# Performance work log

Hardware: AMD Instinct MI355X
Metric: run time of the kernel (lower is better)

The kernel has to match this reference:

```python
import jax, jax.numpy as jnp
import numpy as np

EPS = 1e-5  # config.layer_norm_epsilon

def setup_inputs() -> dict:
    key = jax.random.key(0)
    ks = jax.random.split(key, 8)
    B, S, D, BOT, N = 8, 2048, 1024, 400, 25
    x = jax.random.normal(ks[0], (B, S, D), dtype=jnp.float32)
    alphas = jax.random.uniform(ks[1], (N,), dtype=jnp.float32) / N
    W_down_all = jax.random.normal(ks[2], (N, BOT, D), dtype=jnp.float32) * 0.02
    W_up_all = jax.random.normal(ks[3], (N, D, BOT), dtype=jnp.float32) * 0.02
    b_down_all = jax.random.normal(ks[4], (N, BOT), dtype=jnp.float32) * 0.02
    b_up_all = jax.random.normal(ks[5], (N, D), dtype=jnp.float32) * 0.02
    W_ln_all = 1.0 + jax.random.normal(ks[6], (N, D), dtype=jnp.float32) * 0.02
    b_ln_all = jax.random.normal(ks[7], (N, D), dtype=jnp.float32) * 0.02
    return {"x": x, "alphas": alphas, "W_down_all": W_down_all, "W_up_all": W_up_all,
            "b_down_all": b_down_all, "b_up_all": b_up_all,
            "W_ln_all": W_ln_all, "b_ln_all": b_ln_all}

def reference(x, alphas, W_down_all, W_up_all, b_down_all, b_up_all, W_ln_all, b_ln_all):
    # Superposition: alpha-weighted sum of all adapters' parameters
    # (original python loop over 25 adapters -> single einsum per tensor).
    W_down = jnp.einsum('n,nbd->bd', alphas, W_down_all)  # [BOT, D]
    W_up   = jnp.einsum('n,ndb->db', alphas, W_up_all)    # [D, BOT]
    W_ln   = jnp.einsum('n,nd->d',  alphas, W_ln_all)     # [D]
    b_ln   = jnp.einsum('n,nd->d',  alphas, b_ln_all)     # [D]
    # b_up / b_down are merged in the original too but passed with bias=None: unused.

    # FAdapter: F.layer_norm with normalized_shape = x.shape[1:], i.e. normalize
    # jointly over (seq, embd) per batch element; ln weight/bias broadcast over seq.
    mu = jnp.mean(x, axis=(1, 2), keepdims=True)
    var = jnp.mean(jnp.square(x - mu), axis=(1, 2), keepdims=True)
    x_ = (x - mu) * jax.lax.rsqrt(var + EPS) * W_ln + b_ln  # [B,S,D]

    h = jax.nn.relu(jnp.einsum('bsd,od->bso', x_, W_down))  # [B,S,BOT], no bias
    x_ = jnp.einsum('bso,do->bsd', h, W_up)                 # [B,S,D],   no bias
    return x + x_
```

## Files before the change

kernel.cpp:

```cpp
#include <hip/hip_runtime.h>
#include <stdint.h>

#define NB   8
#define SS   2048
#define DD   1024
#define BOT  400
#define BOTP 512
#define NAD  25
#define LN_EPS 1e-5f
#define NCH  128

typedef __attribute__((ext_vector_type(8))) short bf8_t;
typedef __attribute__((ext_vector_type(4))) float fx4;

__device__ __forceinline__ unsigned short f2bf(float f) {
  unsigned int u = __float_as_uint(f);
  u = (u + 0x7FFFu + ((u >> 16) & 1u)) >> 16;
  return (unsigned short)u;
}
__device__ __forceinline__ uint32_t cvtpk(float lo, float hi) {
  uint32_t r;
  asm("v_cvt_pk_bf16_f32 %0, %1, %2" : "=v"(r) : "v"(lo), "v"(hi));
  return r;
}

__device__ __forceinline__ void gload16(void* lds, const void* g) {
  __builtin_amdgcn_global_load_lds(
      (const __attribute__((address_space(1))) void*)(uintptr_t)g,
      (__attribute__((address_space(3))) void*)(uint32_t)(uintptr_t)lds,
      16, 0, 0);
}

__global__ __launch_bounds__(256) void mixstats_kernel(
    const float* __restrict__ alphas,
    const float* __restrict__ WdAll, const float* __restrict__ WuAll,
    const float* __restrict__ wlnAll, const float* __restrict__ blnAll,
    const float* __restrict__ x,
    unsigned short* __restrict__ Wd, unsigned short* __restrict__ Wu,
    float* __restrict__ wln, float* __restrict__ bln,
    float* __restrict__ partials)
{
  const int tid = threadIdx.x;
  const int bid = blockIdx.x;

  if (bid >= 920) {
    const int g = bid - 920;
    const int b = g >> 7, c = g & 127;
    const float4* xb = (const float4*)(x + (size_t)b * SS * DD) + (size_t)c * 4096;
    float s = 0.f, q = 0.f;
#pragma unroll 4
    for (int i = tid; i < 4096; i += 256) {
      float4 v = xb[i];
      s += v.x + v.y + v.z + v.w;
      q += v.x * v.x + v.y * v.y + v.z * v.z + v.w * v.w;
    }
#pragma unroll
    for (int off = 32; off > 0; off >>= 1) { s += __shfl_down(s, off); q += __shfl_down(q, off); }
    __shared__ float red[8];
    const int wave = tid >> 6, lane = tid & 63;
    if (!lane) { red[wave] = s; red[wave + 4] = q; }
    __syncthreads();
    if (!tid) {
      partials[(b * NCH + c) * 2]     = red[0] + red[1] + red[2] + red[3];
      partials[(b * NCH + c) * 2 + 1] = red[4] + red[5] + red[6] + red[7];
    }
    return;
  }

  __shared__ float a[NAD];
  if (tid < NAD) a[tid] = alphas[tid];
  __syncthreads();

  if (bid < 800) {
    const int g = (bid < 400 ? bid : bid - 400) * 256 + tid;
    const float4* src = (const float4*)(bid < 400 ? WdAll : WuAll) + g;
    float4 vals[NAD];
#pragma unroll
    for (int n = 0; n < NAD; ++n) vals[n] = src[(size_t)n * 102400];
    float4 acc = {0.f, 0.f, 0.f, 0.f};
#pragma unroll
    for (int n = 0; n < NAD; ++n) {
      acc.x += a[n] * vals[n].x; acc.y += a[n] * vals[n].y;
      acc.z += a[n] * vals[n].z; acc.w += a[n] * vals[n].w;
    }
    uint2 pk = { cvtpk(acc.x, acc.y), cvtpk(acc.z, acc.w) };
    if (bid < 400) {
      *(uint2*)(Wd + (size_t)g * 4) = pk;
    } else {
      const int d = g / 100, bg = g - d * 100;
      *(uint2*)(Wu + (size_t)d * BOTP + bg * 4) = pk;
    }
  } else if (bid < 808) {
    const int i = (bid - 800) * 256 + tid;
    const float* src = (i < DD) ? wlnAll : blnAll;
    const int j = (i < DD) ? i : (i - DD);
    float v[NAD];
#pragma unroll
    for (int n = 0; n < NAD; ++n) v[n] = src[(size_t)n * DD + j];
    float s = 0.f;
#pragma unroll
    for (int n = 0; n < NAD; ++n) s += a[n] * v[n];
    if (i < DD) wln[j] = s; else bln[j] = s;
  } else if (bid < 864) {
    const int t = (bid - 808) * 256 + tid;
    int4 z = {0, 0, 0, 0};
    *(int4*)(Wd + 400 * 1024 + (size_t)t * 8) = z;
  } else {
    const int t = (bid - 864) * 256 + tid;
    const int row = t / 14, c8 = t - row * 14;
    int4 z = {0, 0, 0, 0};
    *(int4*)(Wu + (size_t)row * BOTP + 400 + c8 * 8) = z;
  }
}

__global__ __launch_bounds__(256) void gemm1(
    const float* __restrict__ x, const unsigned short* __restrict__ Wdm,
    const float* __restrict__ partials, const float* __restrict__ wln,
    const float* __restrict__ bln, unsigned short* __restrict__ H)
{
  __shared__ char smraw[32768];
  unsigned short* As = (unsigned short*)smraw;
  unsigned short* Bs = (unsigned short*)(smraw + 8192);
  float* s1 = (float*)(smraw + 16384);
  float* s2 = (float*)(smraw + 20480);

  const int tid = threadIdx.x, wave = tid >> 6, lane = tid & 63;
  const int wr = wave >> 1, wc = wave & 1;
  const int bcol = blockIdx.x & 3, brow = blockIdx.x >> 2;
  const int b = brow >> 4;

  double sd = 0.0, qd = 0.0;
#pragma unroll 8
  for (int i = 0; i < NCH; ++i) {
    sd += partials[(b * NCH + i) * 2];
    qd += partials[(b * NCH + i) * 2 + 1];
  }
  const float mu  = (float)(sd * (1.0 / 2097152.0));
  const float var = (float)(qd * (1.0 / 2097152.0)) - mu * mu;
  const float rs  = rsqrtf(var + LN_EPS);
  for (int c = tid; c < DD; c += 256) {
    const float v1 = rs * wln[c];
    s1[c] = v1; s2[c] = bln[c] - mu * v1;
  }

  const float* Ab = x + (size_t)(brow * 128) * DD;
  const unsigned short* Bb = Wdm + (size_t)(bcol * 128) * DD;
  const int row2 = tid >> 1;
  const int c16  = (tid & 1) * 16;

  auto loadA = [&](int k0, float4* xr) {
    const float* p = Ab + (size_t)row2 * DD + k0 + c16;
    xr[0] = *(const float4*)p;     xr[1] = *(const float4*)(p + 4);
    xr[2] = *(const float4*)(p + 8); xr[3] = *(const float4*)(p + 12);
  };
  auto writeA = [&](int k0, const float4* xr) {
    const float4 wA = *(const float4*)&s1[k0 + c16],      wB = *(const float4*)&s1[k0 + c16 + 4];
    const float4 wC = *(const float4*)&s1[k0 + c16 + 8],  wD = *(const float4*)&s1[k0 + c16 + 12];
    const float4 bA = *(const float4*)&s2[k0 + c16],      bB = *(const float4*)&s2[k0 + c16 + 4];
    const float4 bC = *(const float4*)&s2[k0 + c16 + 8],  bD = *(const float4*)&s2[k0 + c16 + 12];
    uint4 p0, p1;
    p0.x = cvtpk(xr[0].x * wA.x + bA.x, xr[0].y * wA.y + bA.y);
    p0.y = cvtpk(xr[0].z * wA.z + bA.z, xr[0].w * wA.w + bA.w);
    p0.z = cvtpk(xr[1].x * wB.x + bB.x, xr[1].y * wB.y + bB.y);
    p0.w = cvtpk(xr[1].z * wB.z + bB.z, xr[1].w * wB.w + bB.w);
    p1.x = cvtpk(xr[2].x * wC.x + bC.x, xr[2].y * wC.y + bC.y);
    p1.y = cvtpk(xr[2].z * wC.z + bC.z, xr[2].w * wC.w + bC.w);
    p1.z = cvtpk(xr[3].x * wD.x + bD.x, xr[3].y * wD.y + bD.y);
    p1.w = cvtpk(xr[3].z * wD.z + bD.z, xr[3].w * wD.w + bD.w);
    *(uint4*)&As[row2 * 32 + c16]     = p0;
    *(uint4*)&As[row2 * 32 + c16 + 8] = p1;
  };
  auto stageB = [&](int k0) {
#pragma unroll
    for (int i = 0; i < 2; ++i) {
      const int basee = (i * 256 + wave * 64) * 8;
      const int e   = basee + lane * 8;
      const int row = e >> 5, col = e & 31;
      gload16(&Bs[basee], Bb + (size_t)row * DD + k0 + col);
    }
  };

  fx4 acc[4][4] = {};
  auto compute = [&]() {
    bf8_t af[4], bf[4];
    const int hi8 = (lane >> 4) * 8;
#pragma unroll
    for (int m = 0; m < 4; ++m)
      af[m] = *(const bf8_t*)&As[(wr * 64 + m * 16 + (lane & 15)) * 32 + hi8];
#pragma unroll
    for (int n = 0; n < 4; ++n)
      bf[n] = *(const bf8_t*)&Bs[(wc * 64 + n * 16 + (lane & 15)) * 32 + hi8];
#pragma unroll
    for (int m = 0; m < 4; ++m)
#pragma unroll
      for (int n = 0; n < 4; ++n)
        acc[m][n] = __builtin_amdgcn_mfma_f32_16x16x32_bf16(af[m], bf[n], acc[m][n], 0, 0, 0);
  };

  float4 xrA[4], xrB[4];
  loadA(0, xrA); stageB(0); loadA(32, xrB);
  __syncthreads();
  writeA(0, xrA);
  __syncthreads();
#pragma unroll 1
  for (int t2 = 0; t2 < 16; ++t2) {
    {
      const int t = t2 * 2;
      compute();
      __syncthreads();
      if (t < 31) {
        stageB((t + 1) * 32);
        writeA((t + 1) * 32, xrB);
        if (t + 2 < 32) loadA((t + 2) * 32, xrA);
      }
      __syncthreads();
    }
    {
      const int t = t2 * 2 + 1;
      compute();
      __syncthreads();
      if (t < 31) {
        stageB((t + 1) * 32);
        writeA((t + 1) * 32, xrA);
        if (t + 2 < 32) loadA((t + 2) * 32, xrB);
      }
      __syncthreads();
    }
  }

  unsigned short* Hs = (unsigned short*)smraw;
  const int r0l = wr * 64 + ((lane >> 4) << 2);
  const int c0l = wc * 64 + (lane & 15);
#pragma unroll
  for (int m = 0; m < 4; ++m)
#pragma unroll
    for (int n = 0; n < 4; ++n)
#pragma unroll
      for (int j = 0; j < 4; ++j) {
        float v = acc[m][n][j];
        Hs[(r0l + m * 16 + j) * 128 + (c0l + n * 16)] = f2bf(v > 0.f ? v : 0.f);
      }
  __syncthreads();
  const size_t outbase = (size_t)(brow * 128) * BOTP + (size_t)bcol * 128;
#pragma unroll
  for (int i = 0; i < 8; ++i) {
    const int idx = i * 256 + tid;
    const int row = idx >> 4, colg = idx & 15;
    *(int4*)(H + outbase + (size_t)row * BOTP + colg * 8) = *(const int4*)&Hs[row * 128 + colg * 8];
  }
}

__global__ __launch_bounds__(256) void gemm2(
    const unsigned short* __restrict__ A, const unsigned short* __restrict__ Bm,
    const float* __restrict__ Xres, float* __restrict__ out)
{
  __shared__ unsigned short As[128 * 32];
  __shared__ unsigned short Bs[128 * 32];
  const int tid = threadIdx.x, wave = tid >> 6, lane = tid & 63;
  const int wr = wave >> 1, wc = wave & 1;
  const int bcol = blockIdx.x & 7, brow = blockIdx.x >> 3;
  const unsigned short* Ab = A + (size_t)(brow * 128) * BOTP;
  const unsigned short* Bb = Bm + (size_t)(bcol * 128) * BOTP;

  fx4 acc[4][4] = {};
  for (int k0 = 0; k0 < 512; k0 += 32) {
#pragma unroll
    for (int i = 0; i < 2; ++i) {
      const int basee = (i * 256 + wave * 64) * 8;
      const int e   = basee + lane * 8;
      const int row = e >> 5, col = e & 31;
      gload16(&As[basee], Ab + (size_t)row * BOTP + k0 + col);
      gload16(&Bs[basee], Bb + (size_t)row * BOTP + k0 + col);
    }
    __syncthreads();
    bf8_t af[4], bf[4];
    const int hi8 = (lane >> 4) * 8;
#pragma unroll
    for (int m = 0; m < 4; ++m)
      af[m] = *(const bf8_t*)&As[(wr * 64 + m * 16 + (lane & 15)) * 32 + hi8];
#pragma unroll
    for (int n = 0; n < 4; ++n)
      bf[n] = *(const bf8_t*)&Bs[(wc * 64 + n * 16 + (lane & 15)) * 32 + hi8];
#pragma unroll
    for (int m = 0; m < 4; ++m)
#pragma unroll
      for (int n = 0; n < 4; ++n)
        acc[m][n] = __builtin_amdgcn_mfma_f32_16x16x32_bf16(af[m], bf[n], acc[m][n], 0, 0, 0);
    __syncthreads();
  }

  const int r0 = brow * 128 + wr * 64 + ((lane >> 4) << 2);
  const int c0 = bcol * 128 + wc * 64 + (lane & 15);
#pragma unroll
  for (int m = 0; m < 4; ++m)
#pragma unroll
    for (int n = 0; n < 4; ++n)
#pragma unroll
      for (int j = 0; j < 4; ++j) {
        const size_t off = (size_t)(r0 + m * 16 + j) * DD + (c0 + n * 16);
        out[off] = acc[m][n][j] + Xres[off];
      }
}

extern "C" void kernel_launch(void* const* d_in, const int* in_sizes, int n_in,
                              void* d_out, int out_size, void* d_ws, size_t ws_size,
                              hipStream_t stream)
{
  const float* x      = (const float*)d_in[0];
  const float* alphas = (const float*)d_in[1];
  const float* WdAll  = (const float*)d_in[2];
  const float* WuAll  = (const float*)d_in[3];
  const float* wlnAll = (const float*)d_in[6];
  const float* blnAll = (const float*)d_in[7];
  float* out = (float*)d_out;

  char* ws = (char*)d_ws;
  unsigned short* Wd  = (unsigned short*)ws;
  unsigned short* Wu  = (unsigned short*)(ws + (1u << 20));
  float* wln          = (float*)(ws + (2u << 20));
  float* bln          = wln + DD;
  float* partials     = bln + DD;
  unsigned short* h   = (unsigned short*)(ws + (3u << 20));

  mixstats_kernel<<<1944, 256, 0, stream>>>(alphas, WdAll, WuAll, wlnAll, blnAll, x,
                                            Wd, Wu, wln, bln, partials);
  gemm1<<<512, 256, 0, stream>>>(x, Wd, partials, wln, bln, h);
  gemm2<<<1024, 256, 0, stream>>>(h, Wu, x, out);
}
```

Baseline: 275.2 us.

## Split layernorm into separate bf16 pass and unify GEMMs with K=64 tiles

LayerNorm application is moved out of gemm1 into a standalone kernel that writes normalized x as bf16 to workspace. Both GEMMs become one templated kernel with 64-wide K tiles, XCD-aware block remapping, and an LDS-staged coalesced epilogue for the fp32 residual add. Sched barriers force all loads to issue before the arithmetic in the mixing and stats kernels. The extra pass writes and rereads about 32 MB of bf16 activations, traded for a simpler GEMM1 inner loop and fewer barriers per K step. The old register double-buffering of A is dropped.

```diff
diff --git a/kernel.cpp b/kernel.cpp
--- a/kernel.cpp
+++ b/kernel.cpp
@@ -47,12 +47,15 @@
     const int g = bid - 920;
     const int b = g >> 7, c = g & 127;
     const float4* xb = (const float4*)(x + (size_t)b * SS * DD) + (size_t)c * 4096;
+    float4 v[16];
+#pragma unroll
+    for (int i = 0; i < 16; ++i) v[i] = xb[i * 256 + tid];
+    __builtin_amdgcn_sched_barrier(0);
     float s = 0.f, q = 0.f;
-#pragma unroll 4
-    for (int i = tid; i < 4096; i += 256) {
-      float4 v = xb[i];
-      s += v.x + v.y + v.z + v.w;
-      q += v.x * v.x + v.y * v.y + v.z * v.z + v.w * v.w;
+#pragma unroll
+    for (int i = 0; i < 16; ++i) {
+      s += v[i].x + v[i].y + v[i].z + v[i].w;
+      q += v[i].x * v[i].x + v[i].y * v[i].y + v[i].z * v[i].z + v[i].w * v[i].w;
     }
 #pragma unroll
     for (int off = 32; off > 0; off >>= 1) { s += __shfl_down(s, off); q += __shfl_down(q, off); }
@@ -77,6 +80,7 @@
     float4 vals[NAD];
 #pragma unroll
     for (int n = 0; n < NAD; ++n) vals[n] = src[(size_t)n * 102400];
+    __builtin_amdgcn_sched_barrier(0);
     float4 acc = {0.f, 0.f, 0.f, 0.f};
 #pragma unroll
     for (int n = 0; n < NAD; ++n) {
@@ -97,6 +101,7 @@
     float v[NAD];
 #pragma unroll
     for (int n = 0; n < NAD; ++n) v[n] = src[(size_t)n * DD + j];
+    __builtin_amdgcn_sched_barrier(0);
     float s = 0.f;
 #pragma unroll
     for (int n = 0; n < NAD; ++n) s += a[n] * v[n];
@@ -113,22 +118,11 @@
   }
 }
 
-__global__ __launch_bounds__(256) void gemm1(
-    const float* __restrict__ x, const unsigned short* __restrict__ Wdm,
+__global__ __launch_bounds__(256) void norm_kernel(const float* __restrict__ x,
     const float* __restrict__ partials, const float* __restrict__ wln,
-    const float* __restrict__ bln, unsigned short* __restrict__ H)
-{
-  __shared__ char smraw[32768];
-  unsigned short* As = (unsigned short*)smraw;
-  unsigned short* Bs = (unsigned short*)(smraw + 8192);
-  float* s1 = (float*)(smraw + 16384);
-  float* s2 = (float*)(smraw + 20480);
-
-  const int tid = threadIdx.x, wave = tid >> 6, lane = tid & 63;
-  const int wr = wave >> 1, wc = wave & 1;
-  const int bcol = blockIdx.x & 3, brow = blockIdx.x >> 2;
-  const int b = brow >> 4;
-
+    const float* __restrict__ bln, unsigned short* __restrict__ xn)
+{
+  const int b = blockIdx.y;
   double sd = 0.0, qd = 0.0;
 #pragma unroll 8
   for (int i = 0; i < NCH; ++i) {
@@ -138,168 +132,126 @@
   const float mu  = (float)(sd * (1.0 / 2097152.0));
   const float var = (float)(qd * (1.0 / 2097152.0)) - mu * mu;
   const float rs  = rsqrtf(var + LN_EPS);
-  for (int c = tid; c < DD; c += 256) {
-    const float v1 = rs * wln[c];
-    s1[c] = v1; s2[c] = bln[c] - mu * v1;
-  }
-
-  const float* Ab = x + (size_t)(brow * 128) * DD;
-  const unsigned short* Bb = Wdm + (size_t)(bcol * 128) * DD;
-  const int row2 = tid >> 1;
-  const int c16  = (tid & 1) * 16;
-
-  auto loadA = [&](int k0, float4* xr) {
-    const float* p = Ab + (size_t)row2 * DD + k0 + c16;
-    xr[0] = *(const float4*)p;     xr[1] = *(const float4*)(p + 4);
-    xr[2] = *(const float4*)(p + 8); xr[3] = *(const float4*)(p + 12);
+
+  const float4* xb = (const float4*)(x + (size_t)b * SS * DD);
+  uint2* xnb = (uint2*)(xn + (size_t)b * SS * DD);
+#pragma unroll
+  for (int it = 0; it < 8; ++it) {
+    const int idx = blockIdx.x * 2048 + it * 256 + threadIdx.x;
+    const int dg = idx & 255;
+    const float4 v = xb[idx];
+    const float4 w = *(const float4*)&wln[dg * 4];
+    const float4 bb = *(const float4*)&bln[dg * 4];
+    const float s1x = rs * w.x, s1y = rs * w.y, s1z = rs * w.z, s1w = rs * w.w;
+    uint2 pk;
+    pk.x = cvtpk((v.x - mu) * s1x + bb.x, (v.y - mu) * s1y + bb.y);
+    pk.y = cvtpk((v.z - mu) * s1z + bb.z, (v.w - mu) * s1w + bb.w);
+    xnb[idx] = pk;
+  }
+}
+
+template <int KDIM, int NBN, bool RELU>
+__global__ __launch_bounds__(256) void gemm_bt(
+    const unsigned short* __restrict__ A, const unsigned short* __restrict__ Bm,
+    const float* __restrict__ Xres, float* __restrict__ Cf,
+    unsigned short* __restrict__ Cb, int N)
+{
+  __shared__ char smraw[32768];
+  unsigned short* As = (unsigned short*)smraw;
+  unsigned short* Bs = (unsigned short*)(smraw + 16384);
+
+  const int tid = threadIdx.x, wave = tid >> 6, lane = tid & 63;
+  const int wr = wave >> 1, wc = wave & 1;
+  const int cpx = gridDim.x >> 3;
+  const int bid = (blockIdx.x & 7) * cpx + (blockIdx.x >> 3);
+  const int bcol = bid & (NBN - 1), brow = bid / NBN;
+  const unsigned short* Ab = A + (size_t)(brow * 128) * KDIM;
+  const unsigned short* Bb = Bm + (size_t)(bcol * 128) * KDIM;
+
+  auto stageM = [&](unsigned short* S, const unsigned short* P, int k0) {
+#pragma unroll
+    for (int i = 0; i < 4; ++i) {
+      const int r = (i & 1) * 64 + wave * 16 + (lane >> 2);
+      const int c = (i >> 1) * 32 + (lane & 3) * 8;
+      gload16(&S[i * 2048 + wave * 512], P + (size_t)r * KDIM + k0 + c);
+    }
   };
-  auto writeA = [&](int k0, const float4* xr) {
-    const float4 wA = *(const float4*)&s1[k0 + c16],      wB = *(const float4*)&s1[k0 + c16 + 4];
-    const float4 wC = *(const float4*)&s1[k0 + c16 + 8],  wD = *(const float4*)&s1[k0 + c16 + 12];
-    const float4 bA = *(const float4*)&s2[k0 + c16],      bB = *(const float4*)&s2[k0 + c16 + 4];
-    const float4 bC = *(const float4*)&s2[k0 + c16 + 8],  bD = *(const float4*)&s2[k0 + c16 + 12];
-    uint4 p0, p1;
-    p0.x = cvtpk(xr[0].x * wA.x + bA.x, xr[0].y * wA.y + bA.y);
-    p0.y = cvtpk(xr[0].z * wA.z + bA.z, xr[0].w * wA.w + bA.w);
-    p0.z = cvtpk(xr[1].x * wB.x + bB.x, xr[1].y * wB.y + bB.y);
-    p0.w = cvtpk(xr[1].z * wB.z + bB.z, xr[1].w * wB.w + bB.w);
-    p1.x = cvtpk(xr[2].x * wC.x + bC.x, xr[2].y * wC.y + bC.y);
-    p1.y = cvtpk(xr[2].z * wC.z + bC.z, xr[2].w * wC.w + bC.w);
-    p1.z = cvtpk(xr[3].x * wD.x + bD.x, xr[3].y * wD.y + bD.y);
-    p1.w = cvtpk(xr[3].z * wD.z + bD.z, xr[3].w * wD.w + bD.w);
-    *(uint4*)&As[row2 * 32 + c16]     = p0;
-    *(uint4*)&As[row2 * 32 + c16 + 8] = p1;
-  };
-  auto stageB = [&](int k0) {
-#pragma unroll
-    for (int i = 0; i < 2; ++i) {
-      const int basee = (i * 256 + wave * 64) * 8;
-      const int e   = basee + lane * 8;
-      const int row = e >> 5, col = e & 31;
-      gload16(&Bs[basee], Bb + (size_t)row * DD + k0 + col);
-    }
-  };
 
   fx4 acc[4][4] = {};
-  auto compute = [&]() {
-    bf8_t af[4], bf[4];
-    const int hi8 = (lane >> 4) * 8;
+#pragma unroll 1
+  for (int t = 0; t < KDIM / 64; ++t) {
+    stageM(As, Ab, t * 64);
+    stageM(Bs, Bb, t * 64);
+    __syncthreads();
+#pragma unroll
+    for (int kk = 0; kk < 2; ++kk) {
+      bf8_t af[4], bf[4];
+      const int ko = kk * 4096 + (lane >> 4) * 8;
+#pragma unroll
+      for (int m = 0; m < 4; ++m)
+        af[m] = *(const bf8_t*)&As[ko + (wr * 64 + m * 16 + (lane & 15)) * 32];
+#pragma unroll
+      for (int n = 0; n < 4; ++n)
+        bf[n] = *(const bf8_t*)&Bs[ko + (wc * 64 + n * 16 + (lane & 15)) * 32];
+#pragma unroll
+      for (int m = 0; m < 4; ++m)
+#pragma unroll
+        for (int n = 0; n < 4; ++n)
+          acc[m][n] = __builtin_amdgcn_mfma_f32_16x16x32_bf16(af[m], bf[n], acc[m][n], 0, 0, 0);
+    }
+    __syncthreads();
+  }
+
+  if constexpr (RELU) {
+    unsigned short* Hs = (unsigned short*)smraw;
+    const int r0l = wr * 64 + ((lane >> 4) << 2);
+    const int c0l = wc * 64 + (lane & 15);
 #pragma unroll
     for (int m = 0; m < 4; ++m)
-      af[m] = *(const bf8_t*)&As[(wr * 64 + m * 16 + (lane & 15)) * 32 + hi8];
-#pragma unroll
-    for (int n = 0; n < 4; ++n)
-      bf[n] = *(const bf8_t*)&Bs[(wc * 64 + n * 16 + (lane & 15)) * 32 + hi8];
-#pragma unroll
-    for (int m = 0; m < 4; ++m)
 #pragma unroll
       for (int n = 0; n < 4; ++n)
-        acc[m][n] = __builtin_amdgcn_mfma_f32_16x16x32_bf16(af[m], bf[n], acc[m][n], 0, 0, 0);
-  };
-
-  float4 xrA[4], xrB[4];
-  loadA(0, xrA); stageB(0); loadA(32, xrB);
-  __syncthreads();
-  writeA(0, xrA);
-  __syncthreads();
-#pragma unroll 1
-  for (int t2 = 0; t2 < 16; ++t2) {
-    {
-      const int t = t2 * 2;
-      compute();
-      __syncthreads();
-      if (t < 31) {
-        stageB((t + 1) * 32);
-        writeA((t + 1) * 32, xrB);
-        if (t + 2 < 32) loadA((t + 2) * 32, xrA);
+#pragma unroll
+        for (int j = 0; j < 4; ++j) {
+          float v = acc[m][n][j];
+          Hs[(r0l + m * 16 + j) * 128 + (c0l + n * 16)] = f2bf(v > 0.f ? v : 0.f);
+        }
+    __syncthreads();
+    const size_t outbase = (size_t)(brow * 128) * N + (size_t)bcol * 128;
+#pragma unroll
+    for (int i = 0; i < 8; ++i) {
+      const int idx = i * 256 + tid;
+      const int row = idx >> 4, colg = idx & 15;
+      *(int4*)(Cb + outbase + (size_t)row * N + colg * 8) = *(const int4*)&Hs[row * 128 + colg * 8];
+    }
+  } else {
+    float* Fs = (float*)smraw;
+#pragma unroll
+    for (int h2 = 0; h2 < 2; ++h2) {
+      if (wr == h2) {
+        const int c0l = wc * 64 + (lane & 15);
+        const int rj = (lane >> 4) << 2;
+#pragma unroll
+        for (int m = 0; m < 4; ++m)
+#pragma unroll
+          for (int n = 0; n < 4; ++n)
+#pragma unroll
+            for (int j = 0; j < 4; ++j)
+              Fs[(m * 16 + rj + j) * 128 + (c0l + n * 16)] = acc[m][n][j];
       }
       __syncthreads();
-    }
-    {
-      const int t = t2 * 2 + 1;
-      compute();
-      __syncthreads();
-      if (t < 31) {
-        stageB((t + 1) * 32);
-        writeA((t + 1) * 32, xrA);
-        if (t + 2 < 32) loadA((t + 2) * 32, xrB);
+      const size_t gb = (size_t)(brow * 128 + h2 * 64) * N + (size_t)bcol * 128;
+#pragma unroll
+      for (int i = 0; i < 8; ++i) {
+        const int idx = i * 256 + tid;
+        const int row = idx >> 5, cg = idx & 31;
+        const float4 f = *(const float4*)&Fs[row * 128 + cg * 4];
+        const float4 xr = *(const float4*)&Xres[gb + (size_t)row * N + cg * 4];
+        float4 o = { f.x + xr.x, f.y + xr.y, f.z + xr.z, f.w + xr.w };
+        *(float4*)&Cf[gb + (size_t)row * N + cg * 4] = o;
       }
       __syncthreads();
     }
   }
-
-  unsigned short* Hs = (unsigned short*)smraw;
-  const int r0l = wr * 64 + ((lane >> 4) << 2);
-  const int c0l = wc * 64 + (lane & 15);
-#pragma unroll
-  for (int m = 0; m < 4; ++m)
-#pragma unroll
-    for (int n = 0; n < 4; ++n)
-#pragma unroll
-      for (int j = 0; j < 4; ++j) {
-        float v = acc[m][n][j];
-        Hs[(r0l + m * 16 + j) * 128 + (c0l + n * 16)] = f2bf(v > 0.f ? v : 0.f);
-      }
-  __syncthreads();
-  const size_t outbase = (size_t)(brow * 128) * BOTP + (size_t)bcol * 128;
-#pragma unroll
-  for (int i = 0; i < 8; ++i) {
-    const int idx = i * 256 + tid;
-    const int row = idx >> 4, colg = idx & 15;
-    *(int4*)(H + outbase + (size_t)row * BOTP + colg * 8) = *(const int4*)&Hs[row * 128 + colg * 8];
-  }
-}
-
-__global__ __launch_bounds__(256) void gemm2(
-    const unsigned short* __restrict__ A, const unsigned short* __restrict__ Bm,
-    const float* __restrict__ Xres, float* __restrict__ out)
-{
-  __shared__ unsigned short As[128 * 32];
-  __shared__ unsigned short Bs[128 * 32];
-  const int tid = threadIdx.x, wave = tid >> 6, lane = tid & 63;
-  const int wr = wave >> 1, wc = wave & 1;
-  const int bcol = blockIdx.x & 7, brow = blockIdx.x >> 3;
-  const unsigned short* Ab = A + (size_t)(brow * 128) * BOTP;
-  const unsigned short* Bb = Bm + (size_t)(bcol * 128) * BOTP;
-
-  fx4 acc[4][4] = {};
-  for (int k0 = 0; k0 < 512; k0 += 32) {
-#pragma unroll
-    for (int i = 0; i < 2; ++i) {
-      const int basee = (i * 256 + wave * 64) * 8;
-      const int e   = basee + lane * 8;
-      const int row = e >> 5, col = e & 31;
-      gload16(&As[basee], Ab + (size_t)row * BOTP + k0 + col);
-      gload16(&Bs[basee], Bb + (size_t)row * BOTP + k0 + col);
-    }
-    __syncthreads();
-    bf8_t af[4], bf[4];
-    const int hi8 = (lane >> 4) * 8;
-#pragma unroll
-    for (int m = 0; m < 4; ++m)
-      af[m] = *(const bf8_t*)&As[(wr * 64 + m * 16 + (lane & 15)) * 32 + hi8];
-#pragma unroll
-    for (int n = 0; n < 4; ++n)
-      bf[n] = *(const bf8_t*)&Bs[(wc * 64 + n * 16 + (lane & 15)) * 32 + hi8];
-#pragma unroll
-    for (int m = 0; m < 4; ++m)
-#pragma unroll
-      for (int n = 0; n < 4; ++n)
-        acc[m][n] = __builtin_amdgcn_mfma_f32_16x16x32_bf16(af[m], bf[n], acc[m][n], 0, 0, 0);
-    __syncthreads();
-  }
-
-  const int r0 = brow * 128 + wr * 64 + ((lane >> 4) << 2);
-  const int c0 = bcol * 128 + wc * 64 + (lane & 15);
-#pragma unroll
-  for (int m = 0; m < 4; ++m)
-#pragma unroll
-    for (int n = 0; n < 4; ++n)
-#pragma unroll
-      for (int j = 0; j < 4; ++j) {
-        const size_t off = (size_t)(r0 + m * 16 + j) * DD + (c0 + n * 16);
-        out[off] = acc[m][n][j] + Xres[off];
-      }
 }
 
 extern "C" void kernel_launch(void* const* d_in, const int* in_sizes, int n_in,
@@ -320,10 +272,12 @@
   float* wln          = (float*)(ws + (2u << 20));
   float* bln          = wln + DD;
   float* partials     = bln + DD;
-  unsigned short* h   = (unsigned short*)(ws + (3u << 20));
+  unsigned short* xn  = (unsigned short*)(ws + (3u << 20));
+  unsigned short* h   = (unsigned short*)(ws + (35u << 20));
 
   mixstats_kernel<<<1944, 256, 0, stream>>>(alphas, WdAll, WuAll, wlnAll, blnAll, x,
                                             Wd, Wu, wln, bln, partials);
-  gemm1<<<512, 256, 0, stream>>>(x, Wd, partials, wln, bln, h);
-  gemm2<<<1024, 256, 0, stream>>>(h, Wu, x, out);
-}
+  norm_kernel<<<dim3(256, NB), 256, 0, stream>>>(x, partials, wln, bln, xn);
+  gemm_bt<1024, 4, true ><<<512,  256, 0, stream>>>(xn, Wd, nullptr, nullptr, h, BOTP);
+  gemm_bt<512,  8, false><<<1024, 256, 0, stream>>>(h, Wu, x, out, nullptr, DD);
+}
```

Measured after the change: 265.2 us. -3.6%, faster.
